# Kernel tuning notes

Measured on AMD Instinct MI355X. Metric: run time of the kernel, lower is better.

The kernel has to match this reference:

```python
import jax, jax.numpy as jnp
import numpy as np

B, L, D, H = 2, 2048, 2048, 16
HD = D // H          # head_dim = 128
LD = HD // 4         # latent_dim = 32


def _linear_params(key, fan_in, fan_out):
    kw, kb = jax.random.split(key)
    bound = 1.0 / np.sqrt(fan_in)
    W = jax.random.uniform(kw, (fan_in, fan_out), jnp.float32, -bound, bound)
    b = jax.random.uniform(kb, (fan_out,), jnp.float32, -bound, bound)
    return W, b


def setup_inputs() -> dict:
    key = jax.random.key(0)
    ks = jax.random.split(key, 12)
    x = jax.random.normal(ks[0], (B, L, D), jnp.float32)
    cos = jax.random.uniform(ks[1], (L, HD // 2), jnp.float32)
    sin = jax.random.uniform(ks[2], (L, HD // 2), jnp.float32)
    Wq, bq = _linear_params(ks[3], D, D)
    Wk, bk = _linear_params(ks[4], D, D)
    Wv, bv = _linear_params(ks[5], D, D)
    Wqc, bqc = _linear_params(ks[6], HD, LD)
    Wkc, bkc = _linear_params(ks[7], HD, LD)
    Wvc, bvc = _linear_params(ks[8], HD, LD)
    Wd, bd = _linear_params(ks[9], LD, HD)
    Wo, bo = _linear_params(ks[10], D, D)
    return dict(x=x, cos=cos, sin=sin, Wq=Wq, bq=bq, Wk=Wk, bk=bk, Wv=Wv, bv=bv,
                Wqc=Wqc, bqc=bqc, Wkc=Wkc, bkc=bkc, Wvc=Wvc, bvc=bvc,
                Wd=Wd, bd=bd, Wo=Wo, bo=bo)


def _apply_rope(q, k, cos, sin):
    # q, k: (B, H, L, HD); cos, sin: (L, HD//2) -> broadcast over B, H
    c = cos[None, None, :, :]
    s = sin[None, None, :, :]
    qe, qo = q[..., ::2], q[..., 1::2]
    ke, ko = k[..., ::2], k[..., 1::2]
    q_rot = jnp.stack([qe * c - qo * s, qe * s + qo * c], axis=-1).reshape(q.shape)
    k_rot = jnp.stack([ke * c - ko * s, ke * s + ko * c], axis=-1).reshape(k.shape)
    return q_rot, k_rot


def reference(x, cos, sin, Wq, bq, Wk, bk, Wv, bv,
              Wqc, bqc, Wkc, bkc, Wvc, bvc, Wd, bd, Wo, bo):
    b, l, d = x.shape
    # projections -> (B, H, L, HD)
    q = (x @ Wq + bq).reshape(b, l, H, HD).transpose(0, 2, 1, 3)
    k = (x @ Wk + bk).reshape(b, l, H, HD).transpose(0, 2, 1, 3)
    v = (x @ Wv + bv).reshape(b, l, H, HD).transpose(0, 2, 1, 3)
    q, k = _apply_rope(q, k, cos, sin)
    # low-rank compression into latent_dim
    qc = jnp.einsum('bhld,de->bhle', q, Wqc) + bqc
    kc = jnp.einsum('bhld,de->bhle', k, Wkc) + bkc
    vc = jnp.einsum('bhld,de->bhle', v, Wvc) + bvc
    scores = jnp.einsum('bhqe,bhke->bhqk', qc, kc) / np.sqrt(LD).astype(np.float32)
    causal = jnp.tril(jnp.ones((l, l), dtype=bool))  # True = keep
    scores = jnp.where(causal[None, None], scores, -jnp.inf)
    probs = jax.nn.softmax(scores, axis=-1)
    attn = jnp.einsum('bhqk,bhke->bhqe', probs, vc)
    attn = jnp.einsum('bhle,ed->bhld', attn, Wd) + bd  # decompress to HD
    attn = attn.transpose(0, 2, 1, 3).reshape(b, l, d)
    return attn @ Wo + bo
```

## Files before the change

kernel.cpp:

```cpp
#include <hip/hip_runtime.h>
#include <hip/hip_bf16.h>


#define Bsz 2
#define Lseq 2048
#define Dmod 2048
#define Hn 16
#define HDim 128
#define LDim 32

typedef __bf16 bf16x8 __attribute__((ext_vector_type(8)));
typedef float f32x4 __attribute__((ext_vector_type(4)));
typedef __hip_bfloat16 bf16;

#define GLDS16(g, l)                                                    \
  __builtin_amdgcn_global_load_lds(                                     \
      (const __attribute__((address_space(1))) unsigned int*)(g),       \
      (__attribute__((address_space(3))) unsigned int*)(l), 16, 0, 0)

#define SM_COS 0
#define SM_SIN 131072
#define SM_WC 262144
#define SM_BC 274432
#define SM_WD 274528
#define SM_BD 278624
#define SM_BO 278752
#define SM_BQKV 280800
#define SM_TOT 286944

__global__ void detect_dtype(const ushort* __restrict__ x, int* __restrict__ flag) {
  int t = threadIdx.x;
  int bad = 0;
  for (int k = 0; k < 4; ++k) {
    ushort u = x[t * 4 + k];
    int ex = (u >> 7) & 0xFF;
    if (ex >= 0xC0) bad = 1;
  }
  unsigned long long b = __ballot(bad);
  if (t == 0) *flag = (b != 0ULL) ? 1 : 0;
}

__device__ inline void conv8(const void* src, size_t so, bf16* dst, size_t dof, int f32) {
  if (f32) {
    const float* s = (const float*)src + so;
    bf16 tmp[8] __attribute__((aligned(16)));
    for (int j = 0; j < 8; ++j) tmp[j] = __float2bfloat16(s[j]);
    *(uint4*)&dst[dof] = *(uint4*)tmp;
  } else {
    *(uint4*)&dst[dof] = *(const uint4*)((const ushort*)src + so);
  }
}

__device__ inline float cv1(const void* s, size_t i, int f32) {
  return f32 ? ((const float*)s)[i] : __bfloat162float(((const bf16*)s)[i]);
}

__global__ __launch_bounds__(256) void conv_x(const void* __restrict__ xs,
                                              bf16* __restrict__ xd,
                                              const int* __restrict__ flagp) {
  int f32 = *flagp;
  size_t e = ((size_t)blockIdx.x * 256 + threadIdx.x) * 8;
  conv8(xs, e, xd, e, f32);
}

__global__ __launch_bounds__(256) void prep(
    const void* cosS, const void* sinS, const void* WqcS, const void* WkcS,
    const void* WvcS, const void* bqcS, const void* bkcS, const void* bvcS,
    const void* WdS, const void* bdS, const void* boS, const void* bqS,
    const void* bkS, const void* bvS, bf16* __restrict__ dst,
    bf16* __restrict__ wctG, bf16* __restrict__ wdtG,
    const int* __restrict__ flagp) {
  int f32 = *flagp;
  int tid = blockIdx.x * 256 + threadIdx.x;
  if (tid < SM_TOT / 8) {
    size_t e = (size_t)tid * 8;
    const void* src;
    size_t so;
    if (e < SM_SIN) { src = cosS; so = e - SM_COS; }
    else if (e < SM_WC) { src = sinS; so = e - SM_SIN; }
    else if (e < SM_BC) { size_t r = e - SM_WC; src = (r < 4096) ? WqcS : (r < 8192) ? WkcS : WvcS; so = r & 4095; }
    else if (e < SM_WD) { size_t r = e - SM_BC; src = (r < 32) ? bqcS : (r < 64) ? bkcS : bvcS; so = r & 31; }
    else if (e < SM_BD) { src = WdS; so = e - SM_WD; }
    else if (e < SM_BO) { src = bdS; so = e - SM_BD; }
    else if (e < SM_BQKV) { src = boS; so = e - SM_BO; }
    else { size_t r = e - SM_BQKV; src = (r < 2048) ? bqS : (r < 4096) ? bkS : bvS; so = r & 2047; }
    conv8(src, so, dst, e, f32);
  } else {
    int idx = tid - SM_TOT / 8;
    for (int i = idx; i < 16384; i += 40960 - SM_TOT / 8) {
      if (i < 12288) {
        int reg = i >> 12, rem = i & 4095, n = rem >> 7, k = rem & 127;
        const void* src = (reg == 0) ? WqcS : (reg == 1) ? WkcS : WvcS;
        wctG[i] = __float2bfloat16(cv1(src, (size_t)k * 32 + n, f32));
      } else {
        int i2 = i - 12288, o = i2 >> 5, e = i2 & 31;
        wdtG[i2] = __float2bfloat16(cv1(WdS, (size_t)e * 128 + o, f32));
      }
    }
  }
}

__global__ __launch_bounds__(256) void transpose4(const void* __restrict__ WqS,
                                                  const void* __restrict__ WkS,
                                                  const void* __restrict__ WvS,
                                                  const void* __restrict__ WoS,
                                                  bf16* __restrict__ WtQKV,
                                                  bf16* __restrict__ WtO,
                                                  const int* __restrict__ flagp) {
  __shared__ float tile[64][65];
  int f32 = *flagp;
  int z = blockIdx.z;
  const void* W = (z == 0) ? WqS : (z == 1) ? WkS : (z == 2) ? WvS : WoS;
  bf16* Wt = (z == 3) ? WtO : (WtQKV + (size_t)z * 2048 * 2048);
  int n0 = blockIdx.x * 64, k0 = blockIdx.y * 64;
  int t = threadIdx.x;
  int x = (t & 7) * 8, y = t >> 3;
  for (int p = 0; p < 2; ++p) {
    int r = y + p * 32;
    if (f32) {
      const float* src = (const float*)W + (size_t)(k0 + r) * 2048 + n0 + x;
      float4 a = *(const float4*)src;
      float4 b2 = *(const float4*)(src + 4);
      tile[r][x + 0] = a.x; tile[r][x + 1] = a.y; tile[r][x + 2] = a.z; tile[r][x + 3] = a.w;
      tile[r][x + 4] = b2.x; tile[r][x + 5] = b2.y; tile[r][x + 6] = b2.z; tile[r][x + 7] = b2.w;
    } else {
      const ushort* src = (const ushort*)W + (size_t)(k0 + r) * 2048 + n0 + x;
      uint4 u = *(const uint4*)src;
      bf16* e = (bf16*)&u;
      for (int j = 0; j < 8; ++j) tile[r][x + j] = __bfloat162float(e[j]);
    }
  }
  __syncthreads();
  for (int p = 0; p < 2; ++p) {
    int n = y + p * 32;
    bf16 tmp[8] __attribute__((aligned(16)));
    for (int j = 0; j < 8; ++j) tmp[j] = __float2bfloat16(tile[x + j][n]);
    *(uint4*)&Wt[(size_t)(n0 + n) * 2048 + k0 + x] = *(uint4*)tmp;
  }
}

#define ESTR 136
__global__ __launch_bounds__(256) void gemm_qkv_compress(
    const bf16* __restrict__ A, const bf16* __restrict__ Bt,
    const bf16* __restrict__ small, const bf16* __restrict__ wctG,
    bf16* __restrict__ qc, bf16* __restrict__ kc, bf16* __restrict__ vcT) {
  __shared__ bf16 sh[128 * ESTR];
  bf16* lA = sh;
  bf16* lB = sh + 4096;
  const int K = 2048;
  int bm = blockIdx.y, bn = blockIdx.x;
  int reg = bn >> 4, h = bn & 15;
  int t = threadIdx.x;
  int lane = t & 63, w = t >> 6;
  int wm = (w >> 1) * 64, wn = (w & 1) * 64;
  int qd = lane >> 4, ln = lane & 15;

  f32x4 acc[4][4] = {};
  const bf16* Ab = A + (size_t)(bm * 128) * K;
  const bf16* Bb = Bt + (size_t)(bn * 128) * K;

  for (int kt = 0; kt < K; kt += 32) {
    for (int p = 0; p < 2; ++p) {
      int slot = t + p * 256;
      int r = slot >> 2, c = (slot & 3) * 8;
      GLDS16(&Ab[(size_t)r * K + kt + c], &lA[slot * 8]);
      GLDS16(&Bb[(size_t)r * K + kt + c], &lB[slot * 8]);
    }
    __syncthreads();
    bf16x8 af[4], bfr[4];
    for (int i = 0; i < 4; ++i) af[i] = *(bf16x8*)&lA[(wm + i * 16 + ln) * 32 + qd * 8];
    for (int j = 0; j < 4; ++j) bfr[j] = *(bf16x8*)&lB[(wn + j * 16 + ln) * 32 + qd * 8];
    for (int i = 0; i < 4; ++i)
      for (int j = 0; j < 4; ++j)
        acc[i][j] = __builtin_amdgcn_mfma_f32_16x16x32_bf16(af[i], bfr[j], acc[i][j], 0, 0, 0);
    __syncthreads();
  }

  for (int j = 0; j < 4; ++j) {
    int col = wn + j * 16 + ln;
    float bv = __bfloat162float(small[SM_BQKV + bn * 128 + col]);
    for (int i = 0; i < 4; ++i)
      for (int r = 0; r < 4; ++r)
        sh[(wm + i * 16 + qd * 4 + r) * ESTR + col] = __float2bfloat16(acc[i][j][r] + bv);
  }
  __syncthreads();

  int r0 = w * 32;
  int b = bm >> 4;
  int bh = b * Hn + h;
  bf16x8 bfr2[2][4];
  for (int nt = 0; nt < 2; ++nt)
    for (int kt = 0; kt < 4; ++kt)
      bfr2[nt][kt] = *(const bf16x8*)&wctG[reg * 4096 + (nt * 16 + ln) * 128 + kt * 32 + qd * 8];
  float bc[2];
  bc[0] = __bfloat162float(small[SM_BC + reg * 32 + ln]);
  bc[1] = __bfloat162float(small[SM_BC + reg * 32 + 16 + ln]);

  for (int mt = 0; mt < 2; ++mt) {
    int lb = r0 + mt * 16 + ln;
    int lg = (bm & 15) * 128 + lb;
    f32x4 c2[2] = {};
    for (int kt = 0; kt < 4; ++kt) {
      uint4 u = *(uint4*)&sh[lb * ESTR + kt * 32 + qd * 8];
      if (reg < 2) {
        bf16* e8 = (bf16*)&u;
        int pbase = kt * 16 + qd * 4;
        for (int j = 0; j < 4; ++j) {
          float cvv = __bfloat162float(small[SM_COS + (size_t)lg * 64 + pbase + j]);
          float svv = __bfloat162float(small[SM_SIN + (size_t)lg * 64 + pbase + j]);
          float ev = __bfloat162float(e8[2 * j]);
          float ov = __bfloat162float(e8[2 * j + 1]);
          e8[2 * j] = __float2bfloat16(ev * cvv - ov * svv);
          e8[2 * j + 1] = __float2bfloat16(ev * svv + ov * cvv);
        }
      }
      bf16x8 a = *(bf16x8*)&u;
      c2[0] = __builtin_amdgcn_mfma_f32_16x16x32_bf16(a, bfr2[0][kt], c2[0], 0, 0, 0);
      c2[1] = __builtin_amdgcn_mfma_f32_16x16x32_bf16(a, bfr2[1][kt], c2[1], 0, 0, 0);
    }
    int lgbase = (bm & 15) * 128 + r0 + mt * 16 + qd * 4;
    if (reg < 2) {
      bf16* dst = (reg == 0) ? qc : kc;
      for (int nt = 0; nt < 2; ++nt)
        for (int r = 0; r < 4; ++r)
          dst[((size_t)bh * Lseq + lgbase + r) * 32 + nt * 16 + ln] =
              __float2bfloat16(c2[nt][r] + bc[nt]);
    } else {
      for (int nt = 0; nt < 2; ++nt) {
        bf16 p4[4] __attribute__((aligned(8)));
        for (int r = 0; r < 4; ++r) p4[r] = __float2bfloat16(c2[nt][r] + bc[nt]);
        *(uint2*)&vcT[((size_t)bh * 32 + nt * 16 + ln) * Lseq + lgbase] = *(uint2*)p4;
      }
    }
  }
}

__global__ __launch_bounds__(256) void gemm_bias_out(const bf16* __restrict__ A,
                                                     const bf16* __restrict__ Bt,
                                                     const bf16* __restrict__ bias,
                                                     void* __restrict__ C,
                                                     int M, int N, int K,
                                                     const int* __restrict__ flagp) {
  __shared__ bf16 lA[128 * 32];
  __shared__ bf16 lB[128 * 32];
  int f32out = *flagp;
  int bm = blockIdx.y, bn = blockIdx.x;
  int t = threadIdx.x;
  int lane = t & 63, w = t >> 6;
  int wm = (w >> 1) * 64, wn = (w & 1) * 64;
  int qd = lane >> 4, ln = lane & 15;

  f32x4 acc[4][4] = {};
  const bf16* Ab = A + (size_t)(bm * 128) * K;
  const bf16* Bb = Bt + (size_t)(bn * 128) * K;

  for (int kt = 0; kt < K; kt += 32) {
    for (int p = 0; p < 2; ++p) {
      int slot = t + p * 256;
      int r = slot >> 2, c = (slot & 3) * 8;
      GLDS16(&Ab[(size_t)r * K + kt + c], &lA[slot * 8]);
      GLDS16(&Bb[(size_t)r * K + kt + c], &lB[slot * 8]);
    }
    __syncthreads();
    bf16x8 af[4], bfr[4];
    for (int i = 0; i < 4; ++i) af[i] = *(bf16x8*)&lA[(wm + i * 16 + ln) * 32 + qd * 8];
    for (int j = 0; j < 4; ++j) bfr[j] = *(bf16x8*)&lB[(wn + j * 16 + ln) * 32 + qd * 8];
    for (int i = 0; i < 4; ++i)
      for (int j = 0; j < 4; ++j)
        acc[i][j] = __builtin_amdgcn_mfma_f32_16x16x32_bf16(af[i], bfr[j], acc[i][j], 0, 0, 0);
    __syncthreads();
  }
  for (int i = 0; i < 4; ++i)
    for (int j = 0; j < 4; ++j) {
      int col = bn * 128 + wn + j * 16 + ln;
      float bv = __bfloat162float(bias[col]);
      for (int r = 0; r < 4; ++r) {
        int row = bm * 128 + wm + i * 16 + qd * 4 + r;
        float v = acc[i][j][r] + bv;
        if (f32out) ((float*)C)[(size_t)row * N + col] = v;
        else ((bf16*)C)[(size_t)row * N + col] = __float2bfloat16(v);
      }
    }
}

__global__ __launch_bounds__(256) void flash32(const bf16* __restrict__ qc,
                                               const bf16* __restrict__ kc,
                                               const bf16* __restrict__ vcT,
                                               const bf16* __restrict__ small,
                                               const bf16* __restrict__ wdtG,
                                               bf16* __restrict__ y) {
  __shared__ bf16 pbuf[4][16 * 40];
  int t = threadIdx.x;
  int lane = t & 63, w = t >> 6;
  int qd = lane >> 4, ln = lane & 15;
  int blk = blockIdx.x;
  int lt = blk & 31;
  int bh = blk >> 5, h = bh & 15, b = bh >> 4;
  int q0 = lt * 64 + w * 16;

  bf16x8 qf = *(const bf16x8*)&qc[((size_t)bh * Lseq + q0 + ln) * 32 + qd * 8];

  f32x4 o0 = {}, o1 = {};
  float m[4], lsum[4];
  for (int r = 0; r < 4; ++r) { m[r] = -1e30f; lsum[r] = 0.f; }
  const float scale = 0.17677669529663687f;

  int nkt = (q0 + 16 + 31) >> 5;
  bf16* pb = pbuf[w];
  for (int kt = 0; kt < nkt; ++kt) {
    int k0 = kt * 32;
    bf16x8 kf0 = *(const bf16x8*)&kc[((size_t)bh * Lseq + k0 + ln) * 32 + qd * 8];
    bf16x8 kf1 = *(const bf16x8*)&kc[((size_t)bh * Lseq + k0 + 16 + ln) * 32 + qd * 8];
    f32x4 s0 = {}, s1 = {};
    s0 = __builtin_amdgcn_mfma_f32_16x16x32_bf16(qf, kf0, s0, 0, 0, 0);
    s1 = __builtin_amdgcn_mfma_f32_16x16x32_bf16(qf, kf1, s1, 0, 0, 0);
    float sv0[4], sv1[4], alpha[4];
    for (int r = 0; r < 4; ++r) {
      int qrow = q0 + qd * 4 + r;
      sv0[r] = (k0 + ln <= qrow) ? s0[r] * scale : -1e30f;
      sv1[r] = (k0 + 16 + ln <= qrow) ? s1[r] * scale : -1e30f;
    }
    for (int r = 0; r < 4; ++r) {
      float mx = fmaxf(sv0[r], sv1[r]);
      for (int off = 1; off < 16; off <<= 1) mx = fmaxf(mx, __shfl_xor(mx, off, 64));
      float mn = fmaxf(m[r], mx);
      alpha[r] = __expf(m[r] - mn);
      m[r] = mn;
      sv0[r] = __expf(sv0[r] - mn);
      sv1[r] = __expf(sv1[r] - mn);
      float rs = sv0[r] + sv1[r];
      for (int off = 1; off < 16; off <<= 1) rs += __shfl_xor(rs, off, 64);
      lsum[r] = lsum[r] * alpha[r] + rs;
      o0[r] *= alpha[r];
      o1[r] *= alpha[r];
    }
    for (int r = 0; r < 4; ++r) {
      pb[(qd * 4 + r) * 40 + ln] = __float2bfloat16(sv0[r]);
      pb[(qd * 4 + r) * 40 + 16 + ln] = __float2bfloat16(sv1[r]);
    }
    asm volatile("s_waitcnt lgkmcnt(0)" ::: "memory");
    bf16x8 pf = *(bf16x8*)&pb[ln * 40 + qd * 8];
    bf16x8 vf0 = *(const bf16x8*)&vcT[((size_t)bh * 32 + ln) * Lseq + k0 + qd * 8];
    bf16x8 vf1 = *(const bf16x8*)&vcT[((size_t)bh * 32 + 16 + ln) * Lseq + k0 + qd * 8];
    o0 = __builtin_amdgcn_mfma_f32_16x16x32_bf16(pf, vf0, o0, 0, 0, 0);
    o1 = __builtin_amdgcn_mfma_f32_16x16x32_bf16(pf, vf1, o1, 0, 0, 0);
  }
  for (int r = 0; r < 4; ++r) {
    float inv = 1.0f / lsum[r];
    pb[(qd * 4 + r) * 40 + ln] = __float2bfloat16(o0[r] * inv);
    pb[(qd * 4 + r) * 40 + 16 + ln] = __float2bfloat16(o1[r] * inv);
  }
  asm volatile("s_waitcnt lgkmcnt(0)" ::: "memory");
  bf16x8 pf = *(bf16x8*)&pb[ln * 40 + qd * 8];
  for (int nt = 0; nt < 8; ++nt) {
    bf16x8 bfr = *(const bf16x8*)&wdtG[(nt * 16 + ln) * 32 + qd * 8];
    f32x4 yacc = {};
    yacc = __builtin_amdgcn_mfma_f32_16x16x32_bf16(pf, bfr, yacc, 0, 0, 0);
    float bb = __bfloat162float(small[SM_BD + nt * 16 + ln]);
    for (int rr = 0; rr < 4; ++rr) {
      int l = q0 + qd * 4 + rr;
      y[(size_t)(b * Lseq + l) * Dmod + h * 128 + nt * 16 + ln] =
          __float2bfloat16(yacc[rr] + bb);
    }
  }
}

extern "C" void kernel_launch(void* const* d_in, const int* in_sizes, int n_in,
                              void* d_out, int out_size, void* d_ws, size_t ws_size,
                              hipStream_t stream) {
  const void* x = d_in[0];
  const void* cosS = d_in[1];
  const void* sinS = d_in[2];
  const void* Wq = d_in[3];
  const void* bq = d_in[4];
  const void* Wk = d_in[5];
  const void* bk = d_in[6];
  const void* Wv = d_in[7];
  const void* bv = d_in[8];
  const void* Wqc = d_in[9];
  const void* bqc = d_in[10];
  const void* Wkc = d_in[11];
  const void* bkc = d_in[12];
  const void* Wvc = d_in[13];
  const void* bvc = d_in[14];
  const void* Wd = d_in[15];
  const void* bd = d_in[16];
  const void* Wo = d_in[17];
  const void* bo = d_in[18];

  char* ws = (char*)d_ws;
  size_t off = 0;
  auto alloc = [&](size_t bytes) {
    char* p = ws + off;
    off += (bytes + 255) & ~(size_t)255;
    return p;
  };
  int* flag = (int*)alloc(256);
  bf16* small = (bf16*)alloc((size_t)SM_TOT * 2);
  bf16* wctG = (bf16*)alloc((size_t)12288 * 2);
  bf16* wdtG = (bf16*)alloc((size_t)4096 * 2);
  bf16* xb = (bf16*)alloc((size_t)4096 * 2048 * 2);
  bf16* WtQKV = (bf16*)alloc((size_t)6144 * 2048 * 2);
  bf16* WtO = (bf16*)alloc((size_t)2048 * 2048 * 2);
  bf16* qcW = (bf16*)alloc((size_t)65536 * 32 * 2);
  bf16* kcW = (bf16*)alloc((size_t)65536 * 32 * 2);
  bf16* vcTW = (bf16*)alloc((size_t)65536 * 32 * 2);
  bf16* yW = (bf16*)alloc((size_t)4096 * 2048 * 2);

  dim3 tb(256);
  detect_dtype<<<1, 64, 0, stream>>>((const ushort*)x, flag);
  prep<<<160, tb, 0, stream>>>(cosS, sinS, Wqc, Wkc, Wvc, bqc, bkc, bvc, Wd, bd, bo, bq,
                               bk, bv, small, wctG, wdtG, flag);
  transpose4<<<dim3(32, 32, 4), tb, 0, stream>>>(Wq, Wk, Wv, Wo, WtQKV, WtO, flag);
  conv_x<<<4096, tb, 0, stream>>>(x, xb, flag);
  gemm_qkv_compress<<<dim3(48, 32), tb, 0, stream>>>(xb, WtQKV, small, wctG, qcW, kcW,
                                                     vcTW);
  flash32<<<1024, tb, 0, stream>>>(qcW, kcW, vcTW, small, wdtG, yW);
  gemm_bias_out<<<dim3(16, 32), tb, 0, stream>>>(yW, WtO, small + SM_BO, d_out, 4096, 2048,
                                                 2048, flag);
}
```

Baseline: 475.3 us.

## Fold V compression into Wv and decompression Wd into Wo projection

Precomputes per-head products Wv·Wvc and Wd·Wo on device, so the V projection directly produces the 32-wide latent and the output GEMM consumes the 512-wide latent attention output with K=512 instead of 2048. This removes the separate V decompress/compress MFMA steps and shrinks the QKV GEMM from 48 to 36 column tiles and the output GEMM's K fourfold. In exchange it adds weight-fold kernels each call, a serial per-thread bias fold loop over 2048 Wo rows, and a different rounding order.

New measurement: 739.8 us. 1.56x slower.

```diff
diff --git a/kernel.cpp b/kernel.cpp
--- a/kernel.cpp
+++ b/kernel.cpp
@@ -100,18 +100,17 @@
   }
 }
 
-__global__ __launch_bounds__(256) void transpose4(const void* __restrict__ WqS,
+__global__ __launch_bounds__(256) void transpose3(const void* __restrict__ WqS,
                                                   const void* __restrict__ WkS,
-                                                  const void* __restrict__ WvS,
                                                   const void* __restrict__ WoS,
-                                                  bf16* __restrict__ WtQKV,
+                                                  bf16* __restrict__ WtQK,
                                                   bf16* __restrict__ WtO,
                                                   const int* __restrict__ flagp) {
   __shared__ float tile[64][65];
   int f32 = *flagp;
   int z = blockIdx.z;
-  const void* W = (z == 0) ? WqS : (z == 1) ? WkS : (z == 2) ? WvS : WoS;
-  bf16* Wt = (z == 3) ? WtO : (WtQKV + (size_t)z * 2048 * 2048);
+  const void* W = (z == 0) ? WqS : (z == 1) ? WkS : WoS;
+  bf16* Wt = (z == 2) ? WtO : (WtQK + (size_t)z * 2048 * 2048);
   int n0 = blockIdx.x * 64, k0 = blockIdx.y * 64;
   int t = threadIdx.x;
   int x = (t & 7) * 8, y = t >> 3;
@@ -139,17 +138,93 @@
   }
 }
 
+__global__ __launch_bounds__(256) void fold_vw(const bf16* __restrict__ WvB,
+                                               const bf16* __restrict__ wctG,
+                                               bf16* __restrict__ Wvt) {
+  int nb = blockIdx.x, h = blockIdx.y;
+  int t = threadIdx.x, lane = t & 63, w = t >> 6;
+  int qd = lane >> 4, ln = lane & 15;
+  f32x4 acc[2][2] = {};
+  for (int kt = 0; kt < 4; ++kt) {
+    bf16x8 af[2], bfr[2];
+    for (int i = 0; i < 2; ++i)
+      af[i] = *(const bf16x8*)&wctG[8192 + (i * 16 + ln) * 128 + kt * 32 + qd * 8];
+    for (int j = 0; j < 2; ++j)
+      bfr[j] = *(const bf16x8*)&WvB[(size_t)(nb * 128 + w * 32 + j * 16 + ln) * 2048 +
+                                    h * 128 + kt * 32 + qd * 8];
+    for (int i = 0; i < 2; ++i)
+      for (int j = 0; j < 2; ++j)
+        acc[i][j] = __builtin_amdgcn_mfma_f32_16x16x32_bf16(af[i], bfr[j], acc[i][j], 0, 0, 0);
+  }
+  for (int i = 0; i < 2; ++i)
+    for (int j = 0; j < 2; ++j)
+      for (int r = 0; r < 4; ++r) {
+        int e = i * 16 + qd * 4 + r;
+        int col = nb * 128 + w * 32 + j * 16 + ln;
+        Wvt[(size_t)(h * 32 + e) * 2048 + col] = __float2bfloat16(acc[i][j][r]);
+      }
+}
+
+__global__ __launch_bounds__(256) void fold_ow(const bf16* __restrict__ WtO,
+                                               const bf16* __restrict__ small,
+                                               bf16* __restrict__ Wot) {
+  int mb = blockIdx.x, h = blockIdx.y;
+  int t = threadIdx.x, lane = t & 63, w = t >> 6;
+  int qd = lane >> 4, ln = lane & 15;
+  f32x4 acc[2][2] = {};
+  for (int kt = 0; kt < 4; ++kt) {
+    bf16x8 af[2], bfr[2];
+    for (int i = 0; i < 2; ++i)
+      af[i] = *(const bf16x8*)&WtO[(size_t)(mb * 128 + w * 32 + i * 16 + ln) * 2048 +
+                                   h * 128 + kt * 32 + qd * 8];
+    for (int j = 0; j < 2; ++j)
+      bfr[j] = *(const bf16x8*)&small[SM_WD + (j * 16 + ln) * 128 + kt * 32 + qd * 8];
+    for (int i = 0; i < 2; ++i)
+      for (int j = 0; j < 2; ++j)
+        acc[i][j] = __builtin_amdgcn_mfma_f32_16x16x32_bf16(af[i], bfr[j], acc[i][j], 0, 0, 0);
+  }
+  for (int i = 0; i < 2; ++i)
+    for (int j = 0; j < 2; ++j)
+      for (int r = 0; r < 4; ++r) {
+        int row = mb * 128 + w * 32 + i * 16 + qd * 4 + r;
+        int col = h * 32 + j * 16 + ln;
+        Wot[(size_t)row * 512 + col] = __float2bfloat16(acc[i][j][r]);
+      }
+}
+
+__global__ __launch_bounds__(256) void fold_bias(const void* boS, const void* bdS,
+                                                 const void* WoS, const void* bvS,
+                                                 const void* bvcS, const void* WvcS,
+                                                 float* __restrict__ boF,
+                                                 float* __restrict__ bvF,
+                                                 const int* __restrict__ flagp) {
+  int f32 = *flagp;
+  int tid = blockIdx.x * 256 + threadIdx.x;
+  if (tid < 2048) {
+    float s = cv1(boS, tid, f32);
+    for (int k = 0; k < 2048; ++k)
+      s += cv1(bdS, k & 127, f32) * cv1(WoS, (size_t)k * 2048 + tid, f32);
+    boF[tid] = s;
+  } else if (tid < 2560) {
+    int j = tid - 2048, h = j >> 5, e = j & 31;
+    float s = cv1(bvcS, e, f32);
+    for (int hd = 0; hd < 128; ++hd)
+      s += cv1(bvS, h * 128 + hd, f32) * cv1(WvcS, (size_t)hd * 32 + e, f32);
+    bvF[j] = s;
+  }
+}
+
 #define ESTR 136
 __global__ __launch_bounds__(256) void gemm_qkv_compress(
     const bf16* __restrict__ A, const bf16* __restrict__ Bt,
-    const bf16* __restrict__ small, const bf16* __restrict__ wctG,
+    const bf16* __restrict__ Wvt, const bf16* __restrict__ small,
+    const bf16* __restrict__ wctG, const float* __restrict__ bvF,
     bf16* __restrict__ qc, bf16* __restrict__ kc, bf16* __restrict__ vcT) {
   __shared__ bf16 sh[128 * ESTR];
   bf16* lA = sh;
   bf16* lB = sh + 4096;
   const int K = 2048;
   int bm = blockIdx.y, bn = blockIdx.x;
-  int reg = bn >> 4, h = bn & 15;
   int t = threadIdx.x;
   int lane = t & 63, w = t >> 6;
   int wm = (w >> 1) * 64, wn = (w & 1) * 64;
@@ -157,7 +232,8 @@
 
   f32x4 acc[4][4] = {};
   const bf16* Ab = A + (size_t)(bm * 128) * K;
-  const bf16* Bb = Bt + (size_t)(bn * 128) * K;
+  const bf16* Bb = (bn < 32) ? (Bt + (size_t)(bn * 128) * K)
+                             : (Wvt + (size_t)((bn - 32) * 128) * K);
 
   for (int kt = 0; kt < K; kt += 32) {
     for (int p = 0; p < 2; ++p) {
@@ -176,6 +252,23 @@
     __syncthreads();
   }
 
+  if (bn >= 32) {
+    int bn2 = bn - 32;
+    int b = bm >> 4;
+    for (int j = 0; j < 4; ++j) {
+      int n = bn2 * 128 + wn + j * 16 + ln;
+      float bb = bvF[n];
+      for (int i = 0; i < 4; ++i) {
+        int lbase = (bm & 15) * 128 + wm + i * 16 + qd * 4;
+        bf16 p4[4] __attribute__((aligned(8)));
+        for (int r = 0; r < 4; ++r) p4[r] = __float2bfloat16(acc[i][j][r] + bb);
+        *(uint2*)&vcT[((size_t)(b * 512 + n)) * 2048 + lbase] = *(uint2*)p4;
+      }
+    }
+    return;
+  }
+
+  int reg = bn >> 4, h = bn & 15;
   for (int j = 0; j < 4; ++j) {
     int col = wn + j * 16 + ln;
     float bv = __bfloat162float(small[SM_BQKV + bn * 128 + col]);
@@ -202,42 +295,32 @@
     f32x4 c2[2] = {};
     for (int kt = 0; kt < 4; ++kt) {
       uint4 u = *(uint4*)&sh[lb * ESTR + kt * 32 + qd * 8];
-      if (reg < 2) {
-        bf16* e8 = (bf16*)&u;
-        int pbase = kt * 16 + qd * 4;
-        for (int j = 0; j < 4; ++j) {
-          float cvv = __bfloat162float(small[SM_COS + (size_t)lg * 64 + pbase + j]);
-          float svv = __bfloat162float(small[SM_SIN + (size_t)lg * 64 + pbase + j]);
-          float ev = __bfloat162float(e8[2 * j]);
-          float ov = __bfloat162float(e8[2 * j + 1]);
-          e8[2 * j] = __float2bfloat16(ev * cvv - ov * svv);
-          e8[2 * j + 1] = __float2bfloat16(ev * svv + ov * cvv);
-        }
+      bf16* e8 = (bf16*)&u;
+      int pbase = kt * 16 + qd * 4;
+      for (int j = 0; j < 4; ++j) {
+        float cvv = __bfloat162float(small[SM_COS + (size_t)lg * 64 + pbase + j]);
+        float svv = __bfloat162float(small[SM_SIN + (size_t)lg * 64 + pbase + j]);
+        float ev = __bfloat162float(e8[2 * j]);
+        float ov = __bfloat162float(e8[2 * j + 1]);
+        e8[2 * j] = __float2bfloat16(ev * cvv - ov * svv);
+        e8[2 * j + 1] = __float2bfloat16(ev * svv + ov * cvv);
       }
       bf16x8 a = *(bf16x8*)&u;
       c2[0] = __builtin_amdgcn_mfma_f32_16x16x32_bf16(a, bfr2[0][kt], c2[0], 0, 0, 0);
       c2[1] = __builtin_amdgcn_mfma_f32_16x16x32_bf16(a, bfr2[1][kt], c2[1], 0, 0, 0);
     }
     int lgbase = (bm & 15) * 128 + r0 + mt * 16 + qd * 4;
-    if (reg < 2) {
-      bf16* dst = (reg == 0) ? qc : kc;
-      for (int nt = 0; nt < 2; ++nt)
-        for (int r = 0; r < 4; ++r)
-          dst[((size_t)bh * Lseq + lgbase + r) * 32 + nt * 16 + ln] =
-              __float2bfloat16(c2[nt][r] + bc[nt]);
-    } else {
-      for (int nt = 0; nt < 2; ++nt) {
-        bf16 p4[4] __attribute__((aligned(8)));
-        for (int r = 0; r < 4; ++r) p4[r] = __float2bfloat16(c2[nt][r] + bc[nt]);
-        *(uint2*)&vcT[((size_t)bh * 32 + nt * 16 + ln) * Lseq + lgbase] = *(uint2*)p4;
-      }
-    }
+    bf16* dst = (reg == 0) ? qc : kc;
+    for (int nt = 0; nt < 2; ++nt)
+      for (int r = 0; r < 4; ++r)
+        dst[((size_t)bh * Lseq + lgbase + r) * 32 + nt * 16 + ln] =
+            __float2bfloat16(c2[nt][r] + bc[nt]);
   }
 }
 
 __global__ __launch_bounds__(256) void gemm_bias_out(const bf16* __restrict__ A,
                                                      const bf16* __restrict__ Bt,
-                                                     const bf16* __restrict__ bias,
+                                                     const float* __restrict__ bias,
                                                      void* __restrict__ C,
                                                      int M, int N, int K,
                                                      const int* __restrict__ flagp) {
@@ -273,7 +356,7 @@
   for (int i = 0; i < 4; ++i)
     for (int j = 0; j < 4; ++j) {
       int col = bn * 128 + wn + j * 16 + ln;
-      float bv = __bfloat162float(bias[col]);
+      float bv = bias[col];
       for (int r = 0; r < 4; ++r) {
         int row = bm * 128 + wm + i * 16 + qd * 4 + r;
         float v = acc[i][j][r] + bv;
@@ -286,9 +369,7 @@
 __global__ __launch_bounds__(256) void flash32(const bf16* __restrict__ qc,
                                                const bf16* __restrict__ kc,
                                                const bf16* __restrict__ vcT,
-                                               const bf16* __restrict__ small,
-                                               const bf16* __restrict__ wdtG,
-                                               bf16* __restrict__ y) {
+                                               bf16* __restrict__ attn) {
   __shared__ bf16 pbuf[4][16 * 40];
   int t = threadIdx.x;
   int lane = t & 63, w = t >> 6;
@@ -347,21 +428,10 @@
   }
   for (int r = 0; r < 4; ++r) {
     float inv = 1.0f / lsum[r];
-    pb[(qd * 4 + r) * 40 + ln] = __float2bfloat16(o0[r] * inv);
-    pb[(qd * 4 + r) * 40 + 16 + ln] = __float2bfloat16(o1[r] * inv);
-  }
-  asm volatile("s_waitcnt lgkmcnt(0)" ::: "memory");
-  bf16x8 pf = *(bf16x8*)&pb[ln * 40 + qd * 8];
-  for (int nt = 0; nt < 8; ++nt) {
-    bf16x8 bfr = *(const bf16x8*)&wdtG[(nt * 16 + ln) * 32 + qd * 8];
-    f32x4 yacc = {};
-    yacc = __builtin_amdgcn_mfma_f32_16x16x32_bf16(pf, bfr, yacc, 0, 0, 0);
-    float bb = __bfloat162float(small[SM_BD + nt * 16 + ln]);
-    for (int rr = 0; rr < 4; ++rr) {
-      int l = q0 + qd * 4 + rr;
-      y[(size_t)(b * Lseq + l) * Dmod + h * 128 + nt * 16 + ln] =
-          __float2bfloat16(yacc[rr] + bb);
-    }
+    int l = q0 + qd * 4 + r;
+    size_t base = ((size_t)(b * Lseq + l)) * 512 + h * 32;
+    attn[base + ln] = __float2bfloat16(o0[r] * inv);
+    attn[base + 16 + ln] = __float2bfloat16(o1[r] * inv);
   }
 }
 
@@ -400,22 +470,31 @@
   bf16* wctG = (bf16*)alloc((size_t)12288 * 2);
   bf16* wdtG = (bf16*)alloc((size_t)4096 * 2);
   bf16* xb = (bf16*)alloc((size_t)4096 * 2048 * 2);
-  bf16* WtQKV = (bf16*)alloc((size_t)6144 * 2048 * 2);
+  bf16* WvB = (bf16*)alloc((size_t)2048 * 2048 * 2);
+  bf16* WtQK = (bf16*)alloc((size_t)4096 * 2048 * 2);
   bf16* WtO = (bf16*)alloc((size_t)2048 * 2048 * 2);
+  bf16* Wvt = (bf16*)alloc((size_t)512 * 2048 * 2);
+  bf16* Wot = (bf16*)alloc((size_t)2048 * 512 * 2);
+  float* boF = (float*)alloc((size_t)2048 * 4);
+  float* bvF = (float*)alloc((size_t)512 * 4);
   bf16* qcW = (bf16*)alloc((size_t)65536 * 32 * 2);
   bf16* kcW = (bf16*)alloc((size_t)65536 * 32 * 2);
   bf16* vcTW = (bf16*)alloc((size_t)65536 * 32 * 2);
-  bf16* yW = (bf16*)alloc((size_t)4096 * 2048 * 2);
+  bf16* attnW = (bf16*)alloc((size_t)4096 * 512 * 2);
 
   dim3 tb(256);
   detect_dtype<<<1, 64, 0, stream>>>((const ushort*)x, flag);
   prep<<<160, tb, 0, stream>>>(cosS, sinS, Wqc, Wkc, Wvc, bqc, bkc, bvc, Wd, bd, bo, bq,
                                bk, bv, small, wctG, wdtG, flag);
-  transpose4<<<dim3(32, 32, 4), tb, 0, stream>>>(Wq, Wk, Wv, Wo, WtQKV, WtO, flag);
+  transpose3<<<dim3(32, 32, 3), tb, 0, stream>>>(Wq, Wk, Wo, WtQK, WtO, flag);
   conv_x<<<4096, tb, 0, stream>>>(x, xb, flag);
-  gemm_qkv_compress<<<dim3(48, 32), tb, 0, stream>>>(xb, WtQKV, small, wctG, qcW, kcW,
-                                                     vcTW);
-  flash32<<<1024, tb, 0, stream>>>(qcW, kcW, vcTW, small, wdtG, yW);
-  gemm_bias_out<<<dim3(16, 32), tb, 0, stream>>>(yW, WtO, small + SM_BO, d_out, 4096, 2048,
-                                                 2048, flag);
-}
+  conv_x<<<2048, tb, 0, stream>>>(Wv, WvB, flag);
+  fold_vw<<<dim3(16, 16), tb, 0, stream>>>(WvB, wctG, Wvt);
+  fold_ow<<<dim3(16, 16), tb, 0, stream>>>(WtO, small, Wot);
+  fold_bias<<<10, tb, 0, stream>>>(bo, bd, Wo, bv, bvc, Wvc, boF, bvF, flag);
+  gemm_qkv_compress<<<dim3(36, 32), tb, 0, stream>>>(xb, WtQK, Wvt, small, wctG, bvF,
+                                                     qcW, kcW, vcTW);
+  flash32<<<1024, tb, 0, stream>>>(qcW, kcW, vcTW, attnW);
+  gemm_bias_out<<<dim3(16, 32), tb, 0, stream>>>(attnW, Wot, boF, d_out, 4096, 2048,
+                                                 512, flag);
+}
```
